# Kernel tuning notes

Hardware: AMD Instinct MI355X
Metric: run time of the kernel (lower is better)

Reference implementation:

```python
import jax, jax.numpy as jnp
import numpy as np

M = 6            # num posenc frequencies
K0 = -3
WIDTH = 128
DEPTH = 7
N_PTS = 131072
N_ANNEAL = 0.6 * 5000.0   # self.N = 0.6 * max_iter
PI = 3.14                 # module uses literal 3.14, not math.pi


def _linear_init(key, fan_in, fan_out):
    k1, k2 = jax.random.split(key)
    lim = 1.0 / np.sqrt(fan_in)
    W = jax.random.uniform(k1, (fan_out, fan_in), jnp.float32, -lim, lim)
    b = jax.random.uniform(k2, (fan_out,), jnp.float32, -lim, lim)
    return W, b


def setup_inputs() -> dict:
    key = jax.random.key(0)
    ks = jax.random.split(key, 11)
    dim_x = M * 6 + 3  # 39
    W_in, b_in = _linear_init(ks[0], dim_x, WIDTH)
    hw, hb = [], []
    for i in range(DEPTH - 1):
        W, b = _linear_init(ks[1 + i], WIDTH, WIDTH)
        hw.append(W)
        hb.append(b)
    Ws, bs = jnp.stack(hw), jnp.stack(hb)  # [6,128,128], [6,128]
    Ww, bw = _linear_init(ks[7], WIDTH, 3)
    Wv, bv = _linear_init(ks[8], WIDTH, 3)
    x = jax.random.normal(ks[9], (N_PTS, 3), jnp.float32)
    return {"x": x, "W_in": W_in, "b_in": b_in, "Ws": Ws, "bs": bs,
            "Ww": Ww, "bw": bw, "Wv": Wv, "bv": bv, "iter": 2500}


def _posenc(pos, it):
    # pos: [N,3]
    j = jnp.arange(M, dtype=pos.dtype)
    a = M * it / N_ANNEAL
    w_a = (1.0 - jnp.cos(jnp.clip(a - j, 0.0, 1.0) * PI)) * 0.5      # [M]
    mul = (2.0 ** (j + K0)) * PI                                     # [M]
    ang = pos[..., :, None] * mul                                    # [N,3,M]
    sin = jnp.sin(ang) * w_a
    cos = jnp.cos(ang) * w_a
    # order: sinx,cosx,siny,cosy,sinz,cosz -> [N,3,2,M] flattened
    code = jnp.stack([sin, cos], axis=-2).reshape(pos.shape[0], 6 * M)
    return jnp.concatenate([pos, code], axis=-1)                     # [N,3+6M]


def _skew(w):
    z = jnp.zeros_like(w[..., 0])
    return jnp.stack([
        jnp.stack([z, -w[..., 2], w[..., 1]], -1),
        jnp.stack([w[..., 2], z, -w[..., 0]], -1),
        jnp.stack([-w[..., 1], w[..., 0], z], -1)], -2)              # [N,3,3]


def _exp_se3(w, v, theta):
    # w,v: [N,3] (axis and v/theta), theta: [N,1]
    W = _skew(w)
    W2 = W @ W
    th = theta[..., None]                                            # [N,1,1]
    s, c = jnp.sin(th), jnp.cos(th)
    I = jnp.eye(3, dtype=w.dtype)
    R = I + s * W + (1.0 - c) * W2
    G = I * th + (1.0 - c) * W + (th - s) * W2
    t = G @ v[..., None]                                             # [N,3,1]
    return R, t


def _warp(x, it, W_in, b_in, Ws, bs, Ww, bw, Wv, bv):
    fea = _posenc(x, it)
    fea = jax.nn.leaky_relu(fea @ W_in.T + b_in, 0.01)

    def layer(f, Wb):
        W, b = Wb
        return jax.nn.relu(f @ W.T + b), None

    fea, _ = jax.lax.scan(layer, fea, (Ws, bs))
    w = fea @ Ww.T + bw
    v = fea @ Wv.T + bv
    theta = jnp.linalg.norm(w, axis=-1, keepdims=True)
    w = w / theta
    v = v / theta
    R, t = _exp_se3(w, v, theta)
    return (R @ x[..., None] + t)[..., 0]                            # [N,3]


def reference(x, W_in, b_in, Ws, bs, Ww, bw, Wv, bv, iter):
    it = float(iter)
    warped = _warp(x, it, W_in, b_in, Ws, bs, Ww, bw, Wv, bv)
    # jacobian of sum over batch -> [3, N, 3]; transpose -> [N, 3, 3]
    f_sum = lambda xx: _warp(xx, it, W_in, b_in, Ws, bs, Ww, bw, Wv, bv).sum(0)
    J = jnp.transpose(jax.jacrev(f_sum)(x), (1, 0, 2))
    return warped, J
```

## Files before the change

kernel.cpp:

```cpp
#include <hip/hip_runtime.h>
#include <math.h>

#define NPTS    131072
#define PPB     64
#define THREADS 256
#define NBLK    (NPTS / PPB)
#define HOFF    (7 * 16384)
#define HSZ     (32 * 128)

typedef __attribute__((ext_vector_type(8)))  short short8;
typedef __attribute__((ext_vector_type(16))) float f32x16;
typedef __attribute__((ext_vector_type(2)))  short s16x2;
typedef __attribute__((ext_vector_type(2)))  __bf16 bf16x2v;

union b8cv { short8 v; unsigned u[4]; };

__device__ __forceinline__ unsigned short f2bf(float f) {
  unsigned u = __float_as_uint(f);
  unsigned r = (u + 0x7fffu + ((u >> 16) & 1u)) >> 16;
  return (unsigned short)r;
}
__device__ __forceinline__ unsigned pk2(float lo, float hi) {
  bf16x2v t;
  t[0] = (__bf16)lo;
  t[1] = (__bf16)hi;
  unsigned u; __builtin_memcpy(&u, &t, 4); return u;
}
__device__ __forceinline__ void gld16(const unsigned short* g, unsigned short* l) {
  __builtin_amdgcn_global_load_lds(
      (const __attribute__((address_space(1))) unsigned int*)(g),
      (__attribute__((address_space(3))) unsigned int*)(l), 16, 0, 0);
}
__device__ __forceinline__ f32x16 zf() {
  f32x16 z;
  #pragma unroll
  for (int e = 0; e < 16; ++e) z[e] = 0.0f;
  return z;
}
__device__ __forceinline__ float qbcast0(float v) {
  return __int_as_float(
      __builtin_amdgcn_mov_dpp(__float_as_int(v), 0x000, 0xf, 0xf, true));
}
__device__ __forceinline__ unsigned relu_pk(unsigned p) {
  unsigned vs = (unsigned)__builtin_amdgcn_mov_dpp((int)p, 0x000, 0xf, 0xf, true);
  s16x2 m2; __builtin_memcpy(&m2, &vs, 4);
  m2 = m2 >> 15;
  unsigned m; __builtin_memcpy(&m, &m2, 4);
  unsigned r;
  asm("v_bfi_b32 %0, %1, 0, %2" : "=v"(r) : "v"(m), "v"(p));
  return r;
}
__device__ __forceinline__ void cross3(const float a[3], const float b[3], float o[3]) {
  o[0] = a[1]*b[2] - a[2]*b[1];
  o[1] = a[2]*b[0] - a[0]*b[2];
  o[2] = a[0]*b[1] - a[1]*b[0];
}
__device__ __forceinline__ float dot3(const float a[3], const float b[3]) {
  return a[0]*b[0] + a[1]*b[1] + a[2]*b[2];
}

__global__ void convert_weights(const float* __restrict__ W_in,
                                const float* __restrict__ b_in,
                                const float* __restrict__ Ws,
                                const float* __restrict__ bs,
                                const float* __restrict__ Ww,
                                const float* __restrict__ Wv,
                                unsigned short* __restrict__ wsW) {
  int idx = blockIdx.x * 256 + threadIdx.x;
  if (idx >= HOFF + HSZ) return;
  float v;
  if (idx < HOFF) {
    int l = idx >> 14, r = idx & 16383, c = r >> 7, k = r & 127;
    if (l == 0) {
      if (k < 39) {
        v = W_in[c * 39 + k];
      } else if (k >= 64 && c < 14) {
        int j  = c * 64 + (k - 64);
        int lb = j >> 7, rr = j & 127;
        int mt = rr >> 5, rd = rr & 31;
        int e2 = rd & 3, hh = (rd >> 2) & 1, q = rd >> 3;
        int src = 32*mt + 16*(q>>1) + 8*hh + 4*(q&1) + e2;
        v = (lb == 0) ? b_in[src] : bs[(lb - 1) * 128 + src];
      } else {
        v = 0.0f;
      }
    } else {
      v = Ws[(l - 1) * 16384 + c * 128 + k];
    }
  } else {
    int r = idx - HOFF, o = r >> 7, k = r & 127;
    v = (o < 3) ? Ww[o * 128 + k] : (o < 6) ? Wv[(o - 3) * 128 + k] : 0.0f;
  }
  wsW[idx] = f2bf(v);
}

__device__ __forceinline__ void dma_full(const unsigned short* __restrict__ g,
                                         unsigned short* lds, int tid) {
  #pragma unroll
  for (int i = 0; i < 8; ++i) {
    int flat = i * 256 + tid;
    int R = flat >> 4, chs = flat & 15, ch = chs ^ (R & 15);
    gld16(g + R * 128 + ch * 8, lds + flat * 8);
  }
}

__device__ __forceinline__ short8 bias_af(const unsigned short* __restrict__ bb,
                                          int off, int c32) {
  b8cv cv;
  cv.u[0] = (unsigned)bb[off + c32];
  cv.u[1] = 0; cv.u[2] = 0; cv.u[3] = 0;
  return cv.v;
}

template <bool LEAKY>
__device__ __forceinline__ void act_pack(const f32x16 (&acc)[2], short8* dst) {
  #pragma unroll
  for (int mt = 0; mt < 2; ++mt)
    #pragma unroll
    for (int qh = 0; qh < 2; ++qh) {
      b8cv cv;
      #pragma unroll
      for (int qs = 0; qs < 2; ++qs) {
        int q = 2*qh + qs;
        if (LEAKY) {
          float pr[4];
          #pragma unroll
          for (int e2 = 0; e2 < 4; ++e2) {
            float post = acc[mt][4*q + e2];
            float vraw = qbcast0(post);
            pr[e2] = vraw > 0.0f ? post : post * 0.01f;
          }
          cv.u[2*qs]     = pk2(pr[0], pr[1]);
          cv.u[2*qs + 1] = pk2(pr[2], pr[3]);
        } else {
          cv.u[2*qs]     = relu_pk(pk2(acc[mt][4*q+0], acc[mt][4*q+1]));
          cv.u[2*qs + 1] = relu_pk(pk2(acc[mt][4*q+2], acc[mt][4*q+3]));
        }
      }
      dst[2*mt + qh] = cv.v;
    }
}

template <int NKS, bool LEAKY, bool HASNEXT>
__device__ __forceinline__ void mlp_layer(short8 (&pgA)[8], short8 (&pgB)[8],
                                          const unsigned short* scur,
                                          unsigned short* snxt,
                                          const int (&aoff)[8],
                                          const unsigned short* __restrict__ bb,
                                          const short8 bind,
                                          const unsigned short* __restrict__ Wnext,
                                          int tid, int c32) {
  if (HASNEXT) dma_full(Wnext, snxt, tid);

  short8 tA[4], tB[4];

  {
    f32x16 aA[2], aB[2];
    #pragma unroll
    for (int m = 0; m < 2; ++m) {
      f32x16 bias = __builtin_amdgcn_mfma_f32_32x32x16_bf16(
          bias_af(bb, 64 + 32*m, c32), bind, zf(), 0, 0, 0);
      short8 af0 = *(const short8*)(scur + m * 4096 + aoff[0]);
      aA[m] = __builtin_amdgcn_mfma_f32_32x32x16_bf16(af0, pgA[0], bias, 0, 0, 0);
      aB[m] = __builtin_amdgcn_mfma_f32_32x32x16_bf16(af0, pgB[0], bias, 0, 0, 0);
    }
    #pragma unroll
    for (int ks = 1; ks < NKS; ++ks) {
      #pragma unroll
      for (int m = 0; m < 2; ++m) {
        short8 af = *(const short8*)(scur + m * 4096 + aoff[ks]);
        aA[m] = __builtin_amdgcn_mfma_f32_32x32x16_bf16(af, pgA[ks], aA[m], 0, 0, 0);
        aB[m] = __builtin_amdgcn_mfma_f32_32x32x16_bf16(af, pgB[ks], aB[m], 0, 0, 0);
      }
    }
    act_pack<LEAKY>(aA, tA);
    act_pack<LEAKY>(aB, tB);
  }

  {
    f32x16 aA[2], aB[2];
    #pragma unroll
    for (int m = 0; m < 2; ++m) {
      f32x16 bias = __builtin_amdgcn_mfma_f32_32x32x16_bf16(
          bias_af(bb, 192 + 32*m, c32), bind, zf(), 0, 0, 0);
      short8 af0 = *(const short8*)(scur + (2 + m) * 4096 + aoff[0]);
      aA[m] = __builtin_amdgcn_mfma_f32_32x32x16_bf16(af0, pgA[0], bias, 0, 0, 0);
      aB[m] = __builtin_amdgcn_mfma_f32_32x32x16_bf16(af0, pgB[0], bias, 0, 0, 0);
    }
    #pragma unroll
    for (int ks = 1; ks < NKS; ++ks) {
      #pragma unroll
      for (int m = 0; m < 2; ++m) {
        short8 af = *(const short8*)(scur + (2 + m) * 4096 + aoff[ks]);
        aA[m] = __builtin_amdgcn_mfma_f32_32x32x16_bf16(af, pgA[ks], aA[m], 0, 0, 0);
        aB[m] = __builtin_amdgcn_mfma_f32_32x32x16_bf16(af, pgB[ks], aB[m], 0, 0, 0);
      }
    }
    act_pack<LEAKY>(aA, &pgA[4]);
    act_pack<LEAKY>(aB, &pgB[4]);
  }

  #pragma unroll
  for (int i = 0; i < 4; ++i) { pgA[i] = tA[i]; pgB[i] = tB[i]; }

  if (HASNEXT) __syncthreads();
}

__device__ __forceinline__ void posenc_pack(const float X[3], int d, int h,
                                            float aM, short8* pg) {
  #pragma unroll
  for (int j = 4; j < 8; ++j) pg[j] = (short8)0;
  #pragma unroll
  for (int j = 0; j < 4; ++j) {
    b8cv cv;
    #pragma unroll
    for (int ii = 0; ii < 4; ++ii) {
      int i = 4*j + ii;
      int mt = i >> 3, rr = i & 7, q = rr >> 1, s = rr & 1;
      int u0 = 32*mt + 16*(q>>1) + 8*h + 4*(q&1) + 2*s;
      float vp[2];
      #pragma unroll
      for (int ci = 0; ci < 2; ++ci) {
        int c = u0 + ci;
        float val = 0.0f;
        if (c < 3) {
          val = (d == 0) ? X[c] : ((c == d - 1) ? 1.0f : 0.0f);
        } else if (c < 39) {
          int kk = c - 3;
          int a  = kk / 12;
          int rm = kk - a * 12;
          int t  = rm / 6;
          int jf = rm - t * 6;
          float e2 = exp2f((float)(jf - 3));
          float mj = e2 * 3.14f;
          float tt = fminf(fmaxf(aM - (float)jf, 0.0f), 1.0f);
          float wj = (1.0f - __builtin_amdgcn_cosf(tt * 0.49974652f)) * 0.5f;
          float rev = X[a] * (e2 * 0.49974652f);
          float fr  = rev - floorf(rev);
          float sv = __builtin_amdgcn_sinf(fr);
          float cvv = __builtin_amdgcn_cosf(fr);
          if (d == 0)          val = (t == 0 ? sv : cvv) * wj;
          else if (a == d - 1) val = (t == 0 ? cvv : -sv) * (mj * wj);
        }
        vp[ci] = val;
      }
      cv.u[ii] = pk2(vp[0], vp[1]);
    }
    pg[j] = cv.v;
  }
}

__global__ __launch_bounds__(THREADS, 2)
void nerfies_mfma(const float* __restrict__ x,
                  const float* __restrict__ bw,
                  const float* __restrict__ bv,
                  const unsigned short* __restrict__ wsW,
                  const int* __restrict__ iterp,
                  float* __restrict__ out)
{
  __shared__ __align__(16) unsigned short sWl[2][128 * 128];
  float* sH = (float*)sWl[1];

  const int tid  = threadIdx.x;
  const int lane = tid & 63;
  const int wv   = tid >> 6;
  const int c32  = lane & 31;
  const int h    = lane >> 5;
  const int p0   = blockIdx.x * PPB;
  const int sig  = (c32 & 0x13) | ((c32 & 4) << 1) | ((c32 & 8) >> 1);

  dma_full(wsW, sWl[0], tid);

  int aoff[8];
  #pragma unroll
  for (int ks = 0; ks < 8; ++ks) aoff[ks] = ((2*ks + h) ^ (sig & 15)) << 3;
  const unsigned short* s0s = sWl[0] + sig * 128;
  const unsigned short* s1s = sWl[1] + sig * 128;

  short8 bind;
  {
    b8cv cv;
    cv.u[0] = ((c32 & 3) == 0) ? 0x3F00u : 0u;
    cv.u[1] = 0; cv.u[2] = 0; cv.u[3] = 0;
    bind = cv.v;
  }

  const int d   = c32 & 3;
  const int gpA = p0 + wv * 16 + (c32 >> 2);
  const int gpB = gpA + 8;
  float XA[3] = { x[gpA * 3 + 0], x[gpA * 3 + 1], x[gpA * 3 + 2] };
  float XB[3] = { x[gpB * 3 + 0], x[gpB * 3 + 1], x[gpB * 3 + 2] };

  int iraw = iterp[0];
  float it = (iraw > 0 && iraw < 100000000) ? (float)iraw : ((const float*)iterp)[0];
  const float aM = 6.0f * it / 3000.0f;

  short8 pgA[8], pgB[8];
  posenc_pack(XA, d, h, aM, pgA);
  posenc_pack(XB, d, h, aM, pgB);
  __syncthreads();

  mlp_layer<3, true , true >(pgA, pgB, s0s, sWl[1], aoff, wsW + 0*256, bind, wsW + 1*16384, tid, c32);
  mlp_layer<8, false, true >(pgA, pgB, s1s, sWl[0], aoff, wsW + 1*256, bind, wsW + 2*16384, tid, c32);
  mlp_layer<8, false, true >(pgA, pgB, s0s, sWl[1], aoff, wsW + 2*256, bind, wsW + 3*16384, tid, c32);
  mlp_layer<8, false, true >(pgA, pgB, s1s, sWl[0], aoff, wsW + 3*256, bind, wsW + 4*16384, tid, c32);
  mlp_layer<8, false, true >(pgA, pgB, s0s, sWl[1], aoff, wsW + 4*256, bind, wsW + 5*16384, tid, c32);
  mlp_layer<8, false, true >(pgA, pgB, s1s, sWl[0], aoff, wsW + 5*256, bind, wsW + 6*16384, tid, c32);
  mlp_layer<8, false, false>(pgA, pgB, s0s, sWl[1], aoff, wsW + 6*256, bind, wsW,           tid, c32);

  {
    const unsigned short* hw = wsW + HOFF;
    short8 af0 = *(const short8*)(hw + c32 * 128 + 8 * h);
    f32x16 hA = __builtin_amdgcn_mfma_f32_32x32x16_bf16(af0, pgA[0], zf(), 0, 0, 0);
    f32x16 hB = __builtin_amdgcn_mfma_f32_32x32x16_bf16(af0, pgB[0], zf(), 0, 0, 0);
    #pragma unroll
    for (int ks = 1; ks < 8; ++ks) {
      short8 afrag = *(const short8*)(hw + c32 * 128 + ks * 16 + 8 * h);
      hA = __builtin_amdgcn_mfma_f32_32x32x16_bf16(afrag, pgA[ks], hA, 0, 0, 0);
      hB = __builtin_amdgcn_mfma_f32_32x32x16_bf16(afrag, pgB[ks], hB, 0, 0, 0);
    }
    int rgA = wv * 64 + c32;
    int rgB = rgA + 32;
    if (h == 0) {
      *(float4*)(sH + rgA * 8) = make_float4(hA[0], hA[1], hA[2], hA[3]);
      *(float4*)(sH + rgB * 8) = make_float4(hB[0], hB[1], hB[2], hB[3]);
    } else {
      *(float2*)(sH + rgA * 8 + 4) = make_float2(hA[0], hA[1]);
      *(float2*)(sH + rgB * 8 + 4) = make_float2(hB[0], hB[1]);
    }
  }
  __syncthreads();

  if (lane < 16) {
    const int p   = lane;
    const int g   = p >> 3, pi = p & 7;
    const int gpp = p0 + wv * 16 + p;
    const int rb  = wv * 64 + g * 32 + pi * 4;
    float XX[3] = { x[gpp*3+0], x[gpp*3+1], x[gpp*3+2] };
    float w[3], v[3], dw[3][3], dv[3][3];
    #pragma unroll
    for (int i = 0; i < 3; ++i) {
      w[i] = sH[rb * 8 + i]     + bw[i];
      v[i] = sH[rb * 8 + 3 + i] + bv[i];
      #pragma unroll
      for (int dd = 0; dd < 3; ++dd) {
        dw[dd][i] = sH[(rb + 1 + dd) * 8 + i];
        dv[dd][i] = sH[(rb + 1 + dd) * 8 + 3 + i];
      }
    }
    float th  = sqrtf(w[0]*w[0] + w[1]*w[1] + w[2]*w[2]);
    float ith = 1.0f / th;
    float u[3]  = { w[0]*ith, w[1]*ith, w[2]*ith };
    float vh[3] = { v[0]*ith, v[1]*ith, v[2]*ith };
    float s = sinf(th), c = cosf(th);
    float C2 = 1.0f - c;
    float ths = th - s;
    float uxx[3]; cross3(u, XX, uxx);
    float udx = dot3(u, XX);
    float uxv[3]; cross3(u, vh, uxv);
    float udv = dot3(u, vh);
    #pragma unroll
    for (int i = 0; i < 3; ++i) {
      float Rx = XX[i] + s * uxx[i] + C2 * (u[i] * udx - XX[i]);
      float tt = th * vh[i] + C2 * uxv[i] + ths * (u[i] * udv - vh[i]);
      out[gpp*3 + i] = Rx + tt;
    }
    float* Jout = out + (size_t)NPTS * 3 + (size_t)gpp * 9;
    #pragma unroll
    for (int dd = 0; dd < 3; ++dd) {
      float dwv[3] = { dw[dd][0], dw[dd][1], dw[dd][2] };
      float dvv[3] = { dv[dd][0], dv[dd][1], dv[dd][2] };
      float dth = dot3(w, dwv) * ith;
      float du[3], dvhv[3];
      #pragma unroll
      for (int i = 0; i < 3; ++i) {
        du[i]   = (dwv[i] - u[i]  * dth) * ith;
        dvhv[i] = (dvv[i] - vh[i] * dth) * ith;
      }
      float ex[3] = { dd == 0 ? 1.0f : 0.0f, dd == 1 ? 1.0f : 0.0f, dd == 2 ? 1.0f : 0.0f };
      float dsv  = c  * dth;
      float dC2  = s  * dth;
      float dths = C2 * dth;
      float duxx[3]; cross3(du, XX, duxx);
      float uxe[3];  cross3(u, ex, uxe);
      float dudx = dot3(du, XX) + u[dd];
      float duxv[3]; cross3(du, vh, duxv);
      float uxdv[3]; cross3(u, dvhv, uxdv);
      float dudv = dot3(du, vh) + dot3(u, dvhv);
      #pragma unroll
      for (int i = 0; i < 3; ++i) {
        float dRx = ex[i] + dsv * uxx[i] + s * (duxx[i] + uxe[i])
                  + dC2 * (u[i] * udx - XX[i])
                  + C2 * (du[i] * udx + u[i] * dudx - ex[i]);
        float dt  = dth * vh[i] + th * dvhv[i] + dC2 * uxv[i]
                  + C2 * (duxv[i] + uxdv[i])
                  + dths * (u[i] * udv - vh[i])
                  + ths * (du[i] * udv + u[i] * dudv - dvhv[i]);
        Jout[i * 3 + dd] = dRx + dt;
      }
    }
  }
}

extern "C" void kernel_launch(void* const* d_in, const int* in_sizes, int n_in,
                              void* d_out, int out_size, void* d_ws, size_t ws_size,
                              hipStream_t stream) {
  const float* x    = (const float*)d_in[0];
  const float* W_in = (const float*)d_in[1];
  const float* b_in = (const float*)d_in[2];
  const float* Ws   = (const float*)d_in[3];
  const float* bs   = (const float*)d_in[4];
  const float* Ww   = (const float*)d_in[5];
  const float* bw   = (const float*)d_in[6];
  const float* Wv   = (const float*)d_in[7];
  const float* bv   = (const float*)d_in[8];
  const int*   itp  = (const int*)d_in[9];
  unsigned short* wsW = (unsigned short*)d_ws;

  convert_weights<<<dim3((HOFF + HSZ + 255) / 256), dim3(256), 0, stream>>>(
      W_in, b_in, Ws, bs, Ww, Wv, wsW);
  nerfies_mfma<<<dim3(NBLK), dim3(THREADS), 0, stream>>>(
      x, bw, bv, wsW, itp, (float*)d_out);
}
```

Measured before the change: 189.2 us.

## Precompute posenc weights, set MFMA priority, spread SE3 epilogue across all lanes

The per-frequency anneal weights and scaled frequencies are computed once per thread, and the posenc slot decode becomes compile-time, so each slot needs only one sin/cos pair selected by the h half. s_setprio raises wave priority around the MFMA accumulation loops so matrix issue is favoured over other waves. The final SE3 warp and Jacobian stage now uses all 64 lanes, with lane groups handling the forward output or one Jacobian column each, instead of 16 lanes doing everything. In exchange, the common exp-map setup is computed redundantly on four lanes per point.

Result: faster. 181.0 us (-4.3%).

```diff
diff --git a/kernel.cpp b/kernel.cpp
--- a/kernel.cpp
+++ b/kernel.cpp
@@ -156,6 +156,7 @@
 
   {
     f32x16 aA[2], aB[2];
+    __builtin_amdgcn_s_setprio(1);
     #pragma unroll
     for (int m = 0; m < 2; ++m) {
       f32x16 bias = __builtin_amdgcn_mfma_f32_32x32x16_bf16(
@@ -173,12 +174,14 @@
         aB[m] = __builtin_amdgcn_mfma_f32_32x32x16_bf16(af, pgB[ks], aB[m], 0, 0, 0);
       }
     }
+    __builtin_amdgcn_s_setprio(0);
     act_pack<LEAKY>(aA, tA);
     act_pack<LEAKY>(aB, tB);
   }
 
   {
     f32x16 aA[2], aB[2];
+    __builtin_amdgcn_s_setprio(1);
     #pragma unroll
     for (int m = 0; m < 2; ++m) {
       f32x16 bias = __builtin_amdgcn_mfma_f32_32x32x16_bf16(
@@ -196,6 +199,7 @@
         aB[m] = __builtin_amdgcn_mfma_f32_32x32x16_bf16(af, pgB[ks], aB[m], 0, 0, 0);
       }
     }
+    __builtin_amdgcn_s_setprio(0);
     act_pack<LEAKY>(aA, &pgA[4]);
     act_pack<LEAKY>(aB, &pgB[4]);
   }
@@ -206,8 +210,33 @@
   if (HASNEXT) __syncthreads();
 }
 
-__device__ __forceinline__ void posenc_pack(const float X[3], int d, int h,
-                                            float aM, short8* pg) {
+struct SK { int cls, a, t, jf; };
+__device__ __forceinline__ constexpr SK slotk(int c) {
+  return (c < 3)   ? SK{1, c, 0, 0}
+       : (c >= 39) ? SK{0, 0, 0, 0}
+       : SK{2, (c-3)/12, ((c-3)%12)/6, ((c-3)%12)%6};
+}
+__device__ __forceinline__ constexpr float e2sf(int jf) {
+  return (float)(1 << jf) * 0.125f * 0.49974652f;
+}
+__device__ __forceinline__ float eval_slot(SK k, const float (&X)[3],
+                                           float sv, float cvv,
+                                           const float (&wjv)[6],
+                                           const float (&mjw)[6],
+                                           float f_d0, const float (&fea)[3]) {
+  if (k.cls == 0) return 0.0f;
+  if (k.cls == 1) return X[k.a] * f_d0 + fea[k.a];
+  float pv = (k.t ? cvv : sv) * wjv[k.jf];
+  float pt = (k.t ? -sv : cvv) * mjw[k.jf];
+  return pv * f_d0 + pt * fea[k.a];
+}
+
+__device__ __forceinline__ void posenc_pack(const float (&X)[3], int h,
+                                            const float (&wjv)[6],
+                                            const float (&mjw)[6],
+                                            float f_d0, const float (&fea)[3],
+                                            short8* pg) {
+  const bool hI = (h != 0);
   #pragma unroll
   for (int j = 4; j < 8; ++j) pg[j] = (short8)0;
   #pragma unroll
@@ -217,32 +246,21 @@
     for (int ii = 0; ii < 4; ++ii) {
       int i = 4*j + ii;
       int mt = i >> 3, rr = i & 7, q = rr >> 1, s = rr & 1;
-      int u0 = 32*mt + 16*(q>>1) + 8*h + 4*(q&1) + 2*s;
+      int u0 = 32*mt + 16*(q>>1) + 4*(q&1) + 2*s;
       float vp[2];
       #pragma unroll
       for (int ci = 0; ci < 2; ++ci) {
-        int c = u0 + ci;
-        float val = 0.0f;
-        if (c < 3) {
-          val = (d == 0) ? X[c] : ((c == d - 1) ? 1.0f : 0.0f);
-        } else if (c < 39) {
-          int kk = c - 3;
-          int a  = kk / 12;
-          int rm = kk - a * 12;
-          int t  = rm / 6;
-          int jf = rm - t * 6;
-          float e2 = exp2f((float)(jf - 3));
-          float mj = e2 * 3.14f;
-          float tt = fminf(fmaxf(aM - (float)jf, 0.0f), 1.0f);
-          float wj = (1.0f - __builtin_amdgcn_cosf(tt * 0.49974652f)) * 0.5f;
-          float rev = X[a] * (e2 * 0.49974652f);
-          float fr  = rev - floorf(rev);
-          float sv = __builtin_amdgcn_sinf(fr);
-          float cvv = __builtin_amdgcn_cosf(fr);
-          if (d == 0)          val = (t == 0 ? sv : cvv) * wj;
-          else if (a == d - 1) val = (t == 0 ? cvv : -sv) * (mj * wj);
-        }
-        vp[ci] = val;
+        const SK k0 = slotk(u0 + ci);
+        const SK k1 = slotk(u0 + ci + 8);
+        float rev0 = (k0.cls == 2) ? X[k0.a] * e2sf(k0.jf) : 0.0f;
+        float rev1 = (k1.cls == 2) ? X[k1.a] * e2sf(k1.jf) : 0.0f;
+        float rev  = hI ? rev1 : rev0;
+        float fr   = rev - floorf(rev);
+        float sv   = __builtin_amdgcn_sinf(fr);
+        float cvv  = __builtin_amdgcn_cosf(fr);
+        float v0 = eval_slot(k0, X, sv, cvv, wjv, mjw, f_d0, fea);
+        float v1 = eval_slot(k1, X, sv, cvv, wjv, mjw, f_d0, fea);
+        vp[ci] = hI ? v1 : v0;
       }
       cv.u[ii] = pk2(vp[0], vp[1]);
     }
@@ -295,9 +313,23 @@
   float it = (iraw > 0 && iraw < 100000000) ? (float)iraw : ((const float*)iterp)[0];
   const float aM = 6.0f * it / 3000.0f;
 
+  float wjv[6], mjw[6];
+  #pragma unroll
+  for (int jf = 0; jf < 6; ++jf) {
+    float e2 = (float)(1 << jf) * 0.125f;
+    float tt = fminf(fmaxf(aM - (float)jf, 0.0f), 1.0f);
+    float wj = (1.0f - __builtin_amdgcn_cosf(tt * 0.49974652f)) * 0.5f;
+    wjv[jf] = wj;
+    mjw[jf] = (e2 * 3.14f) * wj;
+  }
+  const float f_d0 = (d == 0) ? 1.0f : 0.0f;
+  const float fea[3] = { (d == 1) ? 1.0f : 0.0f,
+                         (d == 2) ? 1.0f : 0.0f,
+                         (d == 3) ? 1.0f : 0.0f };
+
   short8 pgA[8], pgB[8];
-  posenc_pack(XA, d, h, aM, pgA);
-  posenc_pack(XB, d, h, aM, pgB);
+  posenc_pack(XA, h, wjv, mjw, f_d0, fea, pgA);
+  posenc_pack(XB, h, wjv, mjw, f_d0, fea, pgB);
   __syncthreads();
 
   mlp_layer<3, true , true >(pgA, pgB, s0s, sWl[1], aoff, wsW + 0*256, bind, wsW + 1*16384, tid, c32);
@@ -331,22 +363,17 @@
   }
   __syncthreads();
 
-  if (lane < 16) {
-    const int p   = lane;
-    const int g   = p >> 3, pi = p & 7;
-    const int gpp = p0 + wv * 16 + p;
-    const int rb  = wv * 64 + g * 32 + pi * 4;
+  {
+    const int pd  = lane & 15;
+    const int sel = lane >> 4;
+    const int gpp = p0 + wv * 16 + pd;
+    const int rb  = wv * 64 + (pd >> 3) * 32 + (pd & 7) * 4;
     float XX[3] = { x[gpp*3+0], x[gpp*3+1], x[gpp*3+2] };
-    float w[3], v[3], dw[3][3], dv[3][3];
+    float w[3], v[3];
     #pragma unroll
     for (int i = 0; i < 3; ++i) {
       w[i] = sH[rb * 8 + i]     + bw[i];
       v[i] = sH[rb * 8 + 3 + i] + bv[i];
-      #pragma unroll
-      for (int dd = 0; dd < 3; ++dd) {
-        dw[dd][i] = sH[(rb + 1 + dd) * 8 + i];
-        dv[dd][i] = sH[(rb + 1 + dd) * 8 + 3 + i];
-      }
     }
     float th  = sqrtf(w[0]*w[0] + w[1]*w[1] + w[2]*w[2]);
     float ith = 1.0f / th;
@@ -359,17 +386,22 @@
     float udx = dot3(u, XX);
     float uxv[3]; cross3(u, vh, uxv);
     float udv = dot3(u, vh);
-    #pragma unroll
-    for (int i = 0; i < 3; ++i) {
-      float Rx = XX[i] + s * uxx[i] + C2 * (u[i] * udx - XX[i]);
-      float tt = th * vh[i] + C2 * uxv[i] + ths * (u[i] * udv - vh[i]);
-      out[gpp*3 + i] = Rx + tt;
-    }
-    float* Jout = out + (size_t)NPTS * 3 + (size_t)gpp * 9;
-    #pragma unroll
-    for (int dd = 0; dd < 3; ++dd) {
-      float dwv[3] = { dw[dd][0], dw[dd][1], dw[dd][2] };
-      float dvv[3] = { dv[dd][0], dv[dd][1], dv[dd][2] };
+    if (sel == 3) {
+      #pragma unroll
+      for (int i = 0; i < 3; ++i) {
+        float Rx = XX[i] + s * uxx[i] + C2 * (u[i] * udx - XX[i]);
+        float tt = th * vh[i] + C2 * uxv[i] + ths * (u[i] * udv - vh[i]);
+        out[gpp*3 + i] = Rx + tt;
+      }
+    } else {
+      const int dd = sel;
+      float* Jout = out + (size_t)NPTS * 3 + (size_t)gpp * 9;
+      float dwv[3], dvv[3];
+      #pragma unroll
+      for (int i = 0; i < 3; ++i) {
+        dwv[i] = sH[(rb + 1 + dd) * 8 + i];
+        dvv[i] = sH[(rb + 1 + dd) * 8 + 3 + i];
+      }
       float dth = dot3(w, dwv) * ith;
       float du[3], dvhv[3];
       #pragma unroll
@@ -378,12 +410,13 @@
         dvhv[i] = (dvv[i] - vh[i] * dth) * ith;
       }
       float ex[3] = { dd == 0 ? 1.0f : 0.0f, dd == 1 ? 1.0f : 0.0f, dd == 2 ? 1.0f : 0.0f };
+      float u_dd  = dd == 0 ? u[0] : (dd == 1 ? u[1] : u[2]);
       float dsv  = c  * dth;
       float dC2  = s  * dth;
       float dths = C2 * dth;
       float duxx[3]; cross3(du, XX, duxx);
       float uxe[3];  cross3(u, ex, uxe);
-      float dudx = dot3(du, XX) + u[dd];
+      float dudx = dot3(du, XX) + u_dd;
       float duxv[3]; cross3(du, vh, duxv);
       float uxdv[3]; cross3(u, dvhv, uxdv);
       float dudv = dot3(du, vh) + dot3(u, dvhv);
```
